# Optimization experiments

Hardware: AMD Instinct MI355X
Metric: run time of the kernel (lower is better)

## Reference

```python
import jax, jax.numpy as jnp
import numpy as np

# Globals from the original script
H_MAX = 10.0
TIMESTEP = 0.01
NUM_SAMPLES = int(H_MAX / TIMESTEP) + 1  # 1001
TRAIN_TD_MAX = 100.0
EMBED_DIM = 32
NUM_NODES = 50000
BATCH = 512


def hawkes_intensity(z_u, z_v, et_uv, td, W, b, psi, alpha, w_t):
    """Faithful to Decoder.hawkes_intensity (symmetric=False branch).
    z_u, z_v: (..., D) broadcastable; et_uv, td broadcastable to output shape.
    The per-event-type masked-linear loop is equivalent to computing both
    1-output linears and selecting by event type.
    """
    D = z_u.shape[-1]
    Wu, Wv = W[:, :D], W[:, D:]  # split Linear(2D -> 1) weights (2, D) each
    et = (et_uv > 0).astype(jnp.int32)
    td_norm = td / TRAIN_TD_MAX
    # g for both event types, broadcast-added instead of materializing cat(z_u, z_v)
    g01 = jnp.matmul(z_u, Wu.T) + jnp.matmul(z_v, Wv.T) + b  # (..., 2)
    g = jnp.where(et == 1, g01[..., 1], g01[..., 0])
    psi_e = psi[et]
    alpha_e = alpha[et]
    w_t_e = w_t[et]
    g = g + alpha_e * jnp.exp(-w_t_e * td_norm)
    g_psi = g / (psi_e + 1e-7)
    # log(1 + exp(-g_psi)) + g_psi, computed stably
    return psi_e * (jnp.logaddexp(0.0, -g_psi) + g_psi)


def setup_inputs() -> dict:
    key = jax.random.key(0)
    ks = jax.random.split(key, 12)
    N, B, D = NUM_NODES, BATCH, EMBED_DIM
    all_embeddings = jax.random.normal(ks[0], (N, D), dtype=jnp.float32)
    assoc = jnp.arange(N, dtype=jnp.int32)  # identity mapping node id -> memory slot
    src = jax.random.randint(ks[1], (B,), 0, N)
    pos_dst = jax.random.randint(ks[2], (B,), 0, N)
    neg_dst = jax.random.randint(ks[3], (B,), 0, N)
    et = jax.random.randint(ks[4], (B,), 0, 2)
    last_update = jax.random.uniform(ks[5], (N,), dtype=jnp.float32) * 50.0
    cur_time = jax.random.uniform(ks[6], (B,), dtype=jnp.float32) * 50.0 + 50.0
    # Linear(2D -> 1) weights for the two event types, stacked: (2, 2D), bias (2,)
    W = jax.random.normal(ks[7], (2, 2 * D), dtype=jnp.float32) / np.sqrt(2 * D)
    b = jax.random.normal(ks[8], (2,), dtype=jnp.float32) * 0.01
    psi = 0.5 * jnp.ones((2,), dtype=jnp.float32)
    alpha = jax.random.uniform(ks[9], (2,), dtype=jnp.float32)
    w_t = jax.random.uniform(ks[10], (2,), dtype=jnp.float32)
    return {"all_embeddings": all_embeddings, "assoc": assoc, "src": src,
            "pos_dst": pos_dst, "neg_dst": neg_dst, "last_update": last_update,
            "cur_time": cur_time, "et": et, "W": W, "b": b, "psi": psi,
            "alpha": alpha, "w_t": w_t}


def reference(all_embeddings, assoc, src, pos_dst, neg_dst, last_update,
              cur_time, et, W, b, psi, alpha, w_t):
    z_src = all_embeddings[assoc[src]]        # (B, D)
    z_dst = all_embeddings[assoc[pos_dst]]    # (B, D)
    td_src = cur_time - last_update[assoc[src]]   # (B,)
    td_dst = cur_time - last_update[assoc[pos_dst]]

    # lambda over all candidate nodes; broadcasting replaces the huge .repeat()
    lambda_src = hawkes_intensity(z_src[:, None, :], all_embeddings[None, :, :],
                                  et[:, None], td_src[:, None],
                                  W, b, psi, alpha, w_t)      # (B, N)
    lambda_dst = hawkes_intensity(all_embeddings[None, :, :], z_dst[:, None, :],
                                  et[:, None], td_dst[:, None],
                                  W, b, psi, alpha, w_t)      # (B, N)

    # return-time prediction via unit-time sampling integral
    all_td = jnp.linspace(0.0, H_MAX, NUM_SAMPLES).astype(jnp.float32)  # (S,)
    # symmetric=True averages two identical calls -> compute once
    intensity = hawkes_intensity(z_src[None, :, :], z_dst[None, :, :],
                                 et[None, :], all_td[:, None],
                                 W, b, psi, alpha, w_t)       # (S, B)
    integral = jnp.cumsum(TIMESTEP * intensity, axis=0)
    density = intensity * jnp.exp(-integral)
    t_sample = all_td[:, None] * density                      # (S, B)
    return_time_pred = (TIMESTEP * 0.5 * (t_sample[:-1] + t_sample[1:])).sum(axis=0)  # (B,)
    return lambda_src, lambda_dst, return_time_pred
```

## Files before the change

kernel.cpp:

```cpp
#include <hip/hip_runtime.h>

#define N_NODES 50000
#define BATCH   512
#define DIM     32
#define LOG2E 1.4426950408889634f
#define LN2   0.6931471805599453f
#define A1C 0.996829f
#define A2C (-0.441666f)
#define A3C 0.139730f

typedef float vfloat4 __attribute__((ext_vector_type(4)));

__global__ void prep_kernel(const float* __restrict__ emb,
                            const int*   __restrict__ assoc,
                            const int*   __restrict__ src,
                            const int*   __restrict__ pdst,
                            const float* __restrict__ last_update,
                            const float* __restrict__ cur_time,
                            const int*   __restrict__ et,
                            const float* __restrict__ W,
                            const float* __restrict__ bias,
                            const float* __restrict__ psi,
                            const float* __restrict__ alpha,
                            const float* __restrict__ w_t,
                            float* __restrict__ nv0, float* __restrict__ nv1,
                            float* __restrict__ nu0, float* __restrict__ nu1,
                            float* __restrict__ pb) {
    if (blockIdx.x < 196) {
        int n = blockIdx.x * 256 + threadIdx.x;
        if (n >= N_NODES) return;
        const float4* e4 = (const float4*)(emb + (size_t)n * DIM);
        float u0 = 0.f, u1 = 0.f, v0 = 0.f, v1 = 0.f;
#pragma unroll
        for (int q = 0; q < 8; ++q) {
            float4 v = e4[q];
            int d = q * 4;
            u0 += v.x * W[d]      + v.y * W[d + 1]      + v.z * W[d + 2]      + v.w * W[d + 3];
            v0 += v.x * W[32 + d] + v.y * W[32 + d + 1] + v.z * W[32 + d + 2] + v.w * W[32 + d + 3];
            u1 += v.x * W[64 + d] + v.y * W[64 + d + 1] + v.z * W[64 + d + 2] + v.w * W[64 + d + 3];
            v1 += v.x * W[96 + d] + v.y * W[96 + d + 1] + v.z * W[96 + d + 2] + v.w * W[96 + d + 3];
        }
        nu0[n] = u0; nu1[n] = u1; nv0[n] = v0; nv1[n] = v1;
    } else {
        int b = (blockIdx.x - 196) * 256 + threadIdx.x;
        if (b >= BATCH) return;
        int e  = (et[b] > 0) ? 1 : 0;
        int is = assoc[src[b]];
        int id = assoc[pdst[b]];
        const float4* Wu = (const float4*)(W + e * 64);
        const float4* Wv = (const float4*)(W + e * 64 + 32);
        const float4* zs = (const float4*)(emb + (size_t)is * DIM);
        const float4* zd = (const float4*)(emb + (size_t)id * DIM);
        float su = 0.f, dv = 0.f;
#pragma unroll
        for (int q = 0; q < 8; ++q) {
            float4 a = zs[q], wa = Wu[q];
            float4 c = zd[q], wc = Wv[q];
            su += a.x * wa.x + a.y * wa.y + a.z * wa.z + a.w * wa.w;
            dv += c.x * wc.x + c.y * wc.y + c.z * wc.z + c.w * wc.w;
        }
        float ct  = cur_time[b];
        float tds = (ct - last_update[is]) * 0.01f;
        float tdd = (ct - last_update[id]) * 0.01f;
        float al = alpha[e], wt = w_t[e], bb = bias[e], ps = psi[e];
        float ip  = 1.0f / (ps + 1e-7f);
        float ipl = ip * LOG2E;
        float bs = su + bb + al * __expf(-wt * tds);
        float bd = dv + bb + al * __expf(-wt * tdd);
        float* p = pb + (size_t)b * 16;
        p[0]  = bs * ipl;
        p[1]  = bd * ipl;
        p[2]  = ipl;
        p[3]  = ps * LN2;
        p[4]  = ps * A1C;
        p[5]  = ps * A2C;
        p[6]  = ps * A3C;
        p[7]  = (float)e;
        p[8]  = su + dv + bb;
        p[9]  = al;
        p[10] = wt;
        p[11] = ps;
        p[12] = ip;
        p[13] = 0.f; p[14] = 0.f; p[15] = 0.f;
    }
}

__global__ void __launch_bounds__(256) main_kernel(
        const float* __restrict__ nv0, const float* __restrict__ nv1,
        const float* __restrict__ nu0, const float* __restrict__ nu1,
        const float* __restrict__ pb,
        float* __restrict__ out) {
    __shared__ float wsum[4];
    __shared__ float bred[4];
    int b = blockIdx.y;
    const float* p = pb + (size_t)b * 16;

    if (blockIdx.x < 49) {
        int n4 = blockIdx.x * 256 + threadIdx.x;
        if (n4 >= N_NODES / 4) return;
        float bsl = p[0], bdl = p[1], ipl = p[2], C1 = p[3];
        float A1p = p[4], A2p = p[5], A3p = p[6];
        int e = (p[7] != 0.f);
        const float4* nvp = (const float4*)(e ? nv1 : nv0);
        const float4* nup = (const float4*)(e ? nu1 : nu0);
        float4 nv = nvp[n4];
        float4 nu = nup[n4];
        auto f = [&](float nvx, float base) {
            float xl = fmaf(nvx, ipl, base);
            float t  = __builtin_amdgcn_exp2f(-fabsf(xl));
            float pp = fmaf(t, A3p, A2p);
            pp = fmaf(t, pp, A1p);
            float m = fmaxf(xl, 0.f);
            return fmaf(pp, t, m * C1);
        };
        vfloat4 os, od;
        os.x = f(nv.x, bsl); os.y = f(nv.y, bsl); os.z = f(nv.z, bsl); os.w = f(nv.w, bsl);
        od.x = f(nu.x, bdl); od.y = f(nu.y, bdl); od.z = f(nu.z, bdl); od.w = f(nu.w, bdl);
        __builtin_nontemporal_store(os, (vfloat4*)(out + (size_t)b * N_NODES) + n4);
        __builtin_nontemporal_store(od, (vfloat4*)(out + (size_t)(BATCH + b) * N_NODES) + n4);
    } else {
        float bint = p[8], al = p[9], wt = p[10], ps = p[11], ip = p[12];
        int tid = threadIdx.x;
        int lane = tid & 63, wv = tid >> 6;
        float inten[4], c[4];
        float cum = 0.f;
#pragma unroll
        for (int i = 0; i < 4; ++i) {
            int t = tid * 4 + i;
            float x = (bint + al * __expf(-wt * (float)t * 1e-4f)) * ip;
            float v = ps * (__logf(1.0f + __expf(-fabsf(x))) + fmaxf(x, 0.0f));
            if (t > 1000) v = 0.f;
            inten[i] = v;
            cum += 0.01f * v;
            c[i] = cum;
        }
        float tot = cum;
#pragma unroll
        for (int off = 1; off < 64; off <<= 1) {
            float u = __shfl_up(tot, off, 64);
            if (lane >= off) tot += u;
        }
        if (lane == 63) wsum[wv] = tot;
        __syncthreads();
        float wpre = 0.f;
#pragma unroll
        for (int w = 0; w < 4; ++w) if (w < wv) wpre += wsum[w];
        float excl = wpre + tot - cum;
        float acc = 0.f;
#pragma unroll
        for (int i = 0; i < 4; ++i) {
            int t = tid * 4 + i;
            float integral = excl + c[i];
            float dens = inten[i] * __expf(-integral);
            float w = (t == 0 || t == 1000) ? 0.005f : (t < 1000 ? 0.01f : 0.f);
            acc += w * (float)t * 0.01f * dens;
        }
#pragma unroll
        for (int off = 32; off > 0; off >>= 1) acc += __shfl_down(acc, off, 64);
        if (lane == 0) bred[wv] = acc;
        __syncthreads();
        if (tid == 0)
            out[(size_t)2 * BATCH * N_NODES + b] = bred[0] + bred[1] + bred[2] + bred[3];
    }
}

extern "C" void kernel_launch(void* const* d_in, const int* in_sizes, int n_in,
                              void* d_out, int out_size, void* d_ws, size_t ws_size,
                              hipStream_t stream) {
    const float* emb         = (const float*)d_in[0];
    const int*   assoc       = (const int*)  d_in[1];
    const int*   src         = (const int*)  d_in[2];
    const int*   pdst        = (const int*)  d_in[3];
    const float* last_update = (const float*)d_in[5];
    const float* cur_time    = (const float*)d_in[6];
    const int*   et          = (const int*)  d_in[7];
    const float* W           = (const float*)d_in[8];
    const float* bias        = (const float*)d_in[9];
    const float* psi         = (const float*)d_in[10];
    const float* alpha       = (const float*)d_in[11];
    const float* w_t         = (const float*)d_in[12];
    float* out = (float*)d_out;

    float* ws  = (float*)d_ws;
    float* nv0 = ws;
    float* nv1 = ws + 50000;
    float* nu0 = ws + 100000;
    float* nu1 = ws + 150000;
    float* pb  = ws + 200000;

    prep_kernel<<<198, 256, 0, stream>>>(emb, assoc, src, pdst, last_update, cur_time,
                                         et, W, bias, psi, alpha, w_t,
                                         nv0, nv1, nu0, nu1, pb);
    dim3 grid(50, BATCH);
    main_kernel<<<grid, 256, 0, stream>>>(nv0, nv1, nu0, nu1, pb, out);
}
```

Measured before the change: 237.5 us.

## Flatten main kernel to a 1D grid over contiguous output float4s

Replaces the 2D (50 x BATCH) grid with a 1D grid where each block writes 512 contiguous float4s of the flattened (2B, N) output, handling src and dst rows through a per-element row/column decode. This removes the partially idle tail block per row and gives fully contiguous, coalesced stores across row boundaries. It also switches from nontemporal stores to ordinary stores, and adds an integer divide plus a per-element parameter load in exchange.

```diff
diff --git a/kernel.cpp b/kernel.cpp
--- a/kernel.cpp
+++ b/kernel.cpp
@@ -3,13 +3,13 @@
 #define N_NODES 50000
 #define BATCH   512
 #define DIM     32
+#define ROW_F4  12500
+#define LBLOCKS 25000
 #define LOG2E 1.4426950408889634f
 #define LN2   0.6931471805599453f
 #define A1C 0.996829f
 #define A2C (-0.441666f)
 #define A3C 0.139730f
-
-typedef float vfloat4 __attribute__((ext_vector_type(4)));
 
 __global__ void prep_kernel(const float* __restrict__ emb,
                             const int*   __restrict__ assoc,
@@ -92,35 +92,43 @@
         float* __restrict__ out) {
     __shared__ float wsum[4];
     __shared__ float bred[4];
-    int b = blockIdx.y;
-    const float* p = pb + (size_t)b * 16;
-
-    if (blockIdx.x < 49) {
-        int n4 = blockIdx.x * 256 + threadIdx.x;
-        if (n4 >= N_NODES / 4) return;
-        float bsl = p[0], bdl = p[1], ipl = p[2], C1 = p[3];
-        float A1p = p[4], A2p = p[5], A3p = p[6];
-        int e = (p[7] != 0.f);
-        const float4* nvp = (const float4*)(e ? nv1 : nv0);
-        const float4* nup = (const float4*)(e ? nu1 : nu0);
-        float4 nv = nvp[n4];
-        float4 nu = nup[n4];
-        auto f = [&](float nvx, float base) {
-            float xl = fmaf(nvx, ipl, base);
-            float t  = __builtin_amdgcn_exp2f(-fabsf(xl));
-            float pp = fmaf(t, A3p, A2p);
-            pp = fmaf(t, pp, A1p);
-            float m = fmaxf(xl, 0.f);
-            return fmaf(pp, t, m * C1);
+    int tid = threadIdx.x;
+
+    if (blockIdx.x < LBLOCKS) {
+        unsigned g0 = blockIdx.x * 512u + (unsigned)tid;
+        auto doit = [&](unsigned g) {
+            unsigned r = g / (unsigned)ROW_F4;
+            unsigned c = g - r * (unsigned)ROW_F4;
+            unsigned b = r & 511u;
+            bool isdst = r >= 512u;
+            const float4* p4 = (const float4*)(pb + (size_t)b * 16);
+            float4 pa = p4[0];
+            float4 pc = p4[1];
+            float base = isdst ? pa.y : pa.x;
+            float ipl = pa.z, C1 = pa.w;
+            float A1p = pc.x, A2p = pc.y, A3p = pc.z;
+            bool e = (pc.w != 0.f);
+            const float4* tab = isdst ? (e ? (const float4*)nu1 : (const float4*)nu0)
+                                      : (e ? (const float4*)nv1 : (const float4*)nv0);
+            float4 nv = tab[c];
+            auto f = [&](float nvx) {
+                float xl = fmaf(nvx, ipl, base);
+                float t  = __builtin_amdgcn_exp2f(-fabsf(xl));
+                float pp = fmaf(t, A3p, A2p);
+                pp = fmaf(t, pp, A1p);
+                float m = fmaxf(xl, 0.f);
+                return fmaf(pp, t, m * C1);
+            };
+            float4 o;
+            o.x = f(nv.x); o.y = f(nv.y); o.z = f(nv.z); o.w = f(nv.w);
+            ((float4*)out)[g] = o;
         };
-        vfloat4 os, od;
-        os.x = f(nv.x, bsl); os.y = f(nv.y, bsl); os.z = f(nv.z, bsl); os.w = f(nv.w, bsl);
-        od.x = f(nu.x, bdl); od.y = f(nu.y, bdl); od.z = f(nu.z, bdl); od.w = f(nu.w, bdl);
-        __builtin_nontemporal_store(os, (vfloat4*)(out + (size_t)b * N_NODES) + n4);
-        __builtin_nontemporal_store(od, (vfloat4*)(out + (size_t)(BATCH + b) * N_NODES) + n4);
+        doit(g0);
+        doit(g0 + 256u);
     } else {
+        int b = blockIdx.x - LBLOCKS;
+        const float* p = pb + (size_t)b * 16;
         float bint = p[8], al = p[9], wt = p[10], ps = p[11], ip = p[12];
-        int tid = threadIdx.x;
         int lane = tid & 63, wv = tid >> 6;
         float inten[4], c[4];
         float cum = 0.f;
@@ -191,6 +199,5 @@
     prep_kernel<<<198, 256, 0, stream>>>(emb, assoc, src, pdst, last_update, cur_time,
                                          et, W, bias, psi, alpha, w_t,
                                          nv0, nv1, nu0, nu1, pb);
-    dim3 grid(50, BATCH);
-    main_kernel<<<grid, 256, 0, stream>>>(nv0, nv1, nu0, nu1, pb, out);
+    main_kernel<<<LBLOCKS + BATCH, 256, 0, stream>>>(nv0, nv1, nu0, nu1, pb, out);
 }
```

Measured after the change: 272.5 us. 1.15x slower.
